# Performance work log

Hardware: AMD Instinct MI355X
Metric: run time of the kernel (lower is better)

## Reference

```python
import jax, jax.numpy as jnp
import numpy as np
import math

BS, LQ, LKV = 4, 2048, 2048
D_LATENT, D_MODEL, HEADS = 512, 512, 8
D_K = D_MODEL // HEADS


def setup_inputs() -> dict:
    key = jax.random.key(0)
    ks = jax.random.split(key, 12)
    s = 0.02
    return {
        "q": jax.random.normal(ks[0], (BS, LQ, D_LATENT), jnp.float32),
        "k": jax.random.normal(ks[1], (BS, LKV, D_MODEL), jnp.float32),
        "v": jax.random.normal(ks[2], (BS, LKV, D_MODEL), jnp.float32),
        "weights": jax.random.uniform(ks[3], (BS, LKV), jnp.float32) + 1e-3,
        "Wq": jax.random.normal(ks[4], (D_LATENT, D_MODEL), jnp.float32) * s,
        "bq": jnp.zeros((D_MODEL,), jnp.float32),
        "Wk": jax.random.normal(ks[5], (D_MODEL, D_MODEL), jnp.float32) * s,
        "bk": jnp.zeros((D_MODEL,), jnp.float32),
        "Wv": jax.random.normal(ks[6], (D_MODEL, D_MODEL), jnp.float32) * s,
        "bv": jnp.zeros((D_MODEL,), jnp.float32),
        "Wo": jax.random.normal(ks[7], (D_MODEL, D_MODEL), jnp.float32) * s,
        "bo": jnp.zeros((D_MODEL,), jnp.float32),
    }


def reference(q, k, v, weights, Wq, bq, Wk, bk, Wv, bv, Wo, bo):
    bs = q.shape[0]
    # QKV projections, split into heads: [bs, h, L, d_k]
    qh = (q @ Wq + bq).reshape(bs, -1, HEADS, D_K).transpose(0, 2, 1, 3)
    kh = (k @ Wk + bk).reshape(bs, -1, HEADS, D_K).transpose(0, 2, 1, 3)
    vh = (v @ Wv + bv).reshape(bs, -1, HEADS, D_K).transpose(0, 2, 1, 3)
    # scaled dot-product scores [bs, h, Lq, Lkv]
    scores = jnp.einsum("bhqd,bhkd->bhqk", qh, kh) / math.sqrt(D_K)
    p = jax.nn.softmax(scores, axis=-1)
    # post-softmax external weight renormalization
    wp = p * weights[:, None, None, :]
    wp = wp / wp.sum(-1, keepdims=True)
    out = jnp.einsum("bhqk,bhkd->bhqd", wp, vh)
    concat = out.transpose(0, 2, 1, 3).reshape(bs, -1, D_MODEL)
    return concat @ Wo + bo
```

## Files before the change

### kernel.cpp

```cpp
#include <hip/hip_runtime.h>
#include <hip/hip_bf16.h>

#define LQ 2048
#define LKV 2048
#define DM 512
#define NH 8
#define DK 64

typedef __attribute__((ext_vector_type(8))) __bf16 bf16x8;
typedef __attribute__((ext_vector_type(4))) float f32x4;
typedef __attribute__((ext_vector_type(16))) float f32x16;

#define AS1 __attribute__((address_space(1)))
#define AS3 __attribute__((address_space(3)))

static __device__ __forceinline__ unsigned short f2bf(float x) {
  unsigned u = __float_as_uint(x);
  return (unsigned short)((u + 0x7fffu + ((u >> 16) & 1u)) >> 16);
}
static __device__ __forceinline__ float bf2f(unsigned short u) {
  return __uint_as_float(((unsigned)u) << 16);
}
static __device__ __forceinline__ bf16x8 cvt8(f32x4 a, f32x4 b) {
  bf16x8 r;
  r[0] = (__bf16)a[0]; r[1] = (__bf16)a[1]; r[2] = (__bf16)a[2]; r[3] = (__bf16)a[3];
  r[4] = (__bf16)b[0]; r[5] = (__bf16)b[1]; r[6] = (__bf16)b[2]; r[7] = (__bf16)b[3];
  return r;
}

__global__ __launch_bounds__(256) void transpose_w(
    const float* __restrict__ Wq, const float* __restrict__ Wk,
    const float* __restrict__ Wv, const float* __restrict__ Wo,
    unsigned short* __restrict__ WtAll)
{
  const float* W = blockIdx.z == 0 ? Wq : blockIdx.z == 1 ? Wk : blockIdx.z == 2 ? Wv : Wo;
  unsigned short* Wt = WtAll + (size_t)blockIdx.z * DM * DM;
  __shared__ float tile[32][33];
  const int t = threadIdx.x;
  const int tr = t >> 3;
  const int tc4 = (t & 7) * 4;
  const int k0 = blockIdx.x * 32, n0 = blockIdx.y * 32;
  float4 v = *(const float4*)(W + (size_t)(k0 + tr) * DM + n0 + tc4);
  tile[tr][tc4 + 0] = v.x; tile[tr][tc4 + 1] = v.y;
  tile[tr][tc4 + 2] = v.z; tile[tr][tc4 + 3] = v.w;
  __syncthreads();
  ushort4 o;
  o.x = f2bf(tile[tc4 + 0][tr]);
  o.y = f2bf(tile[tc4 + 1][tr]);
  o.z = f2bf(tile[tc4 + 2][tr]);
  o.w = f2bf(tile[tc4 + 3][tr]);
  *(ushort4*)(Wt + (size_t)(n0 + tr) * DM + k0 + tc4) = o;
}

__global__ __launch_bounds__(256) void gemm_qkv(
    const float* __restrict__ qin, const float* __restrict__ kin, const float* __restrict__ vin,
    const unsigned short* __restrict__ WtAll,
    const float* __restrict__ bq, const float* __restrict__ bk, const float* __restrict__ bv,
    unsigned short* __restrict__ qh, unsigned short* __restrict__ kh, unsigned short* __restrict__ vh)
{
  const int bid = blockIdx.x;
  const int x = bid & 7, j = bid >> 3;
  const int p = x + 8 * (j >> 2);
  const int nt = j & 3;
  const int mode = p >> 6, mtile = p & 63;

  const float* A = mode == 0 ? qin : (mode == 1 ? kin : vin);
  const unsigned short* Bt = WtAll + (size_t)mode * DM * DM;
  const float* bias = mode == 0 ? bq : (mode == 1 ? bk : bv);
  unsigned short* out = mode == 0 ? qh : (mode == 1 ? kh : vh);
  const float scale = (mode == 0) ? 0.18033688011112042f : 1.0f;

  __shared__ __align__(16) float As[128 * 32];
  __shared__ __align__(16) unsigned short Bs[128 * 32];

  const int tid = threadIdx.x;
  const int lane = tid & 63;
  const int w = tid >> 6;
  const int wr = w >> 1, wc = w & 1;
  const int l15 = lane & 15, g = lane >> 4;
  const int m0 = mtile * 128, n0 = nt * 128;

  f32x4 acc[4][4] = {};

  for (int k0 = 0; k0 < DM; k0 += 32) {
#pragma unroll
    for (int i = 0; i < 4; ++i) {
      int c = tid + i * 256;
      int row = c >> 3, slot = c & 7;
      const float* src = A + (size_t)(m0 + row) * DM + k0 + ((slot ^ (row & 7)) << 2);
      __builtin_amdgcn_global_load_lds((const AS1 unsigned*)src,
                                       (AS3 unsigned*)((char*)As + c * 16), 16, 0, 0);
    }
#pragma unroll
    for (int i = 0; i < 2; ++i) {
      int c = tid + i * 256;
      int row = c >> 2, slot = c & 3;
      const unsigned short* src = Bt + (size_t)(n0 + row) * DM + k0 + ((slot ^ ((row >> 1) & 3)) * 8);
      __builtin_amdgcn_global_load_lds((const AS1 unsigned*)src,
                                       (AS3 unsigned*)((char*)Bs + c * 16), 16, 0, 0);
    }
    __syncthreads();

    bf16x8 af[4], bfr[4];
#pragma unroll
    for (int mi = 0; mi < 4; ++mi) {
      int row = wr * 64 + mi * 16 + l15;
      f32x4 a0 = *(const f32x4*)((const char*)As + row * 128 + (((2 * g) ^ (row & 7)) << 4));
      f32x4 a1 = *(const f32x4*)((const char*)As + row * 128 + (((2 * g + 1) ^ (row & 7)) << 4));
      af[mi] = cvt8(a0, a1);
    }
#pragma unroll
    for (int ni = 0; ni < 4; ++ni) {
      int row = wc * 64 + ni * 16 + l15;
      bfr[ni] = *(const bf16x8*)((const char*)Bs + row * 64 + ((g ^ ((row >> 1) & 3)) * 16));
    }
#pragma unroll
    for (int mi = 0; mi < 4; ++mi)
#pragma unroll
      for (int ni = 0; ni < 4; ++ni)
        acc[mi][ni] = __builtin_amdgcn_mfma_f32_16x16x32_bf16(af[mi], bfr[ni], acc[mi][ni], 0, 0, 0);
    __syncthreads();
  }

#pragma unroll
  for (int mi = 0; mi < 4; ++mi) {
#pragma unroll
    for (int ni = 0; ni < 4; ++ni) {
      int n = n0 + wc * 64 + ni * 16 + l15;
      float bs = bias[n];
      int h = n >> 6, d = n & 63;
#pragma unroll
      for (int r = 0; r < 4; ++r) {
        int m = m0 + wr * 64 + mi * 16 + g * 4 + r;
        int b = m >> 11, li = m & 2047;
        float val = (acc[mi][ni][r] + bs) * scale;
        out[(((size_t)(b * NH + h)) * LQ + li) * DK + d] = f2bf(val);
      }
    }
  }
}

__global__ __launch_bounds__(256) void gemm_out(
    const unsigned short* __restrict__ A, const unsigned short* __restrict__ Bt,
    const float* __restrict__ bias, float* __restrict__ out)
{
  __shared__ __align__(16) unsigned short Al[128 * 40];
  __shared__ __align__(16) unsigned short Bl[128 * 40];
  const int tid = threadIdx.x;
  const int lane = tid & 63;
  const int w = tid >> 6;
  const int wr = w >> 1, wc = w & 1;
  const int l15 = lane & 15, g = lane >> 4;
  const int m0 = blockIdx.x * 128, n0 = blockIdx.y * 128;
  f32x4 acc[4][4] = {};

  for (int k0 = 0; k0 < DM; k0 += 32) {
#pragma unroll
    for (int i = 0; i < 2; ++i) {
      int idx = tid + i * 256;
      int row = idx >> 2, seg = idx & 3;
      *(int4*)(&Al[row * 40 + seg * 8]) =
          *(const int4*)(A + (size_t)(m0 + row) * DM + k0 + seg * 8);
      *(int4*)(&Bl[row * 40 + seg * 8]) =
          *(const int4*)(Bt + (size_t)(n0 + row) * DM + k0 + seg * 8);
    }
    __syncthreads();
    bf16x8 af[4], bfr[4];
#pragma unroll
    for (int mi = 0; mi < 4; ++mi)
      af[mi] = *(const bf16x8*)(&Al[(wr * 64 + mi * 16 + l15) * 40 + g * 8]);
#pragma unroll
    for (int ni = 0; ni < 4; ++ni)
      bfr[ni] = *(const bf16x8*)(&Bl[(wc * 64 + ni * 16 + l15) * 40 + g * 8]);
#pragma unroll
    for (int mi = 0; mi < 4; ++mi)
#pragma unroll
      for (int ni = 0; ni < 4; ++ni)
        acc[mi][ni] = __builtin_amdgcn_mfma_f32_16x16x32_bf16(af[mi], bfr[ni], acc[mi][ni], 0, 0, 0);
    __syncthreads();
  }

#pragma unroll
  for (int mi = 0; mi < 4; ++mi) {
#pragma unroll
    for (int ni = 0; ni < 4; ++ni) {
      int n = n0 + wc * 64 + ni * 16 + l15;
      float bs = bias[n];
#pragma unroll
      for (int r = 0; r < 4; ++r) {
        int m = m0 + wr * 64 + mi * 16 + g * 4 + r;
        out[(size_t)m * DM + n] = acc[mi][ni][r] + bs;
      }
    }
  }
}

__global__ __launch_bounds__(256) void prep_kv(
    const unsigned short* __restrict__ kh, const unsigned short* __restrict__ vh,
    const float* __restrict__ wts,
    unsigned short* __restrict__ kf, unsigned short* __restrict__ vf,
    unsigned short* __restrict__ wbf)
{
  __shared__ __align__(16) unsigned short t[64 * 72];
  const int bh = blockIdx.y, l0 = blockIdx.x * 64;
  const int b = bh >> 3;
  const size_t base = (size_t)bh * LKV * DK;
  const int tid = threadIdx.x;

  if ((bh & 7) == 0 && tid < 64)
    wbf[b * LKV + l0 + tid] = f2bf(wts[b * LKV + l0 + tid]);

#pragma unroll
  for (int i = 0; i < 2; ++i) {
    int c = tid + i * 256;
    int sl = c & 63, cq = (c >> 6) & 3, tl = c >> 8;
    int kv = tl * 32 + (sl & 31);
    int4 blk = *(const int4*)(kh + base + (size_t)(l0 + kv) * DK + cq * 16 + (sl >> 5) * 8);
    *(int4*)(kf + base + ((((size_t)(l0 >> 5) + tl) * 4 + cq) * 64 + sl) * 8) = blk;
  }

#pragma unroll
  for (int i = 0; i < 2; ++i) {
    int idx = tid + i * 256;
    int row = idx >> 3, seg = idx & 7;
    *(int4*)(&t[row * 72 + seg * 8]) =
        *(const int4*)(vh + base + (size_t)(l0 + row) * DK + seg * 8);
  }
  __syncthreads();
#pragma unroll
  for (int i = 0; i < 2; ++i) {
    int idx = tid + i * 256;
    int d = idx >> 3, seg = idx & 7;
    int kvg = l0 + seg * 8;
    float4 wa = *(const float4*)(wts + b * LKV + kvg);
    float4 wb = *(const float4*)(wts + b * LKV + kvg + 4);
    unsigned short r0 = f2bf(wa.x * bf2f(t[(seg * 8 + 0) * 72 + d]));
    unsigned short r1 = f2bf(wa.y * bf2f(t[(seg * 8 + 1) * 72 + d]));
    unsigned short r2 = f2bf(wa.z * bf2f(t[(seg * 8 + 2) * 72 + d]));
    unsigned short r3 = f2bf(wa.w * bf2f(t[(seg * 8 + 3) * 72 + d]));
    unsigned short r4 = f2bf(wb.x * bf2f(t[(seg * 8 + 4) * 72 + d]));
    unsigned short r5 = f2bf(wb.y * bf2f(t[(seg * 8 + 5) * 72 + d]));
    unsigned short r6 = f2bf(wb.z * bf2f(t[(seg * 8 + 6) * 72 + d]));
    unsigned short r7 = f2bf(wb.w * bf2f(t[(seg * 8 + 7) * 72 + d]));
    int4 o;
    o.x = (int)((unsigned)r0 | ((unsigned)r1 << 16));
    o.y = (int)((unsigned)r2 | ((unsigned)r3 << 16));
    o.z = (int)((unsigned)r4 | ((unsigned)r5 << 16));
    o.w = (int)((unsigned)r6 | ((unsigned)r7 << 16));
    size_t addr = ((((size_t)bh * 128 + (kvg >> 4)) * 2 + (d >> 5)) * 64 +
                   ((d & 31) + ((kvg >> 3) & 1) * 32)) * 8;
    *(int4*)(vf + addr) = o;
  }
}

__global__ __launch_bounds__(512, 4) void attn_fwd(
    const unsigned short* __restrict__ qh, const unsigned short* __restrict__ kf,
    const unsigned short* __restrict__ vf, const unsigned short* __restrict__ wbf,
    unsigned short* __restrict__ ao)
{
  const int bid = blockIdx.x;
  const int xcd = bid & 7, wi = bid >> 3;
  const int bh = xcd * 4 + (wi >> 4);
  const int qb = wi & 15;
  const int b = bh >> 3, h = bh & 7;
  const int tid = threadIdx.x, lane = tid & 63, w = tid >> 6;
  const int wq = w & 3, half = w >> 2;
  const int l31 = lane & 31, hi = lane >> 5;

  __shared__ __align__(16) char smem[36864];

  const size_t kv_bh = (size_t)bh * (LKV * DK);
  const unsigned short* kfb = kf + kv_bh;
  const unsigned short* vfb = vf + kv_bh;

  const int q0 = qb * 128 + wq * 32;

#define STAGE(buf, t)                                                                     \
  do {                                                                                    \
    int tg_ = half * 32 + (t);                                                            \
    const unsigned short* ks_ = kfb + ((size_t)(tg_ * 4 + wq) * 64 + lane) * 8;           \
    const unsigned short* vs_ = vfb + ((size_t)((tg_ * 2 + (wq >> 1)) * 2 + (wq & 1)) * 64 + lane) * 8; \
    char* kd_ = smem + (buf) * 16384 + half * 8192 + wq * 1024;                           \
    char* vd_ = smem + (buf) * 16384 + half * 8192 + 4096 + wq * 1024;                    \
    __builtin_amdgcn_global_load_lds((const AS1 unsigned*)ks_, (AS3 unsigned*)kd_, 16, 0, 0); \
    __builtin_amdgcn_global_load_lds((const AS1 unsigned*)vs_, (AS3 unsigned*)vd_, 16, 0, 0); \
  } while (0)

  if (tid < 256)
    __builtin_amdgcn_global_load_lds((const AS1 unsigned*)(wbf + b * LKV + tid * 8),
                                     (AS3 unsigned*)(smem + 32768 + tid * 16), 16, 0, 0);
  STAGE(0, 0);

  bf16x8 qf[4];
  {
    const unsigned short* qp = qh + kv_bh + (size_t)(q0 + l31) * DK + hi * 8;
#pragma unroll
    for (int cq = 0; cq < 4; ++cq) qf[cq] = *(const bf16x8*)(qp + cq * 16);
  }
  asm volatile("s_waitcnt vmcnt(0)" ::: "memory");
  __builtin_amdgcn_s_barrier();

  const char* wl = smem + 32768 + half * 2048;
  f32x16 accO0 = {}, accO1 = {}, accL = {};
  int cur = 0;

#pragma unroll 2
  for (int t = 0; t < 32; ++t) {
    if (t < 31) {
      STAGE(cur ^ 1, t + 1);
      asm volatile("s_waitcnt vmcnt(2)" ::: "memory");
    } else {
      asm volatile("s_waitcnt vmcnt(0)" ::: "memory");
    }
    __builtin_amdgcn_s_barrier();

    const char* Kb = smem + cur * 16384 + half * 8192;
    const char* Vb = Kb + 4096;

    __builtin_amdgcn_s_setprio(1);
    f32x16 s = {};
#pragma unroll
    for (int cq = 0; cq < 4; ++cq) {
      bf16x8 kfr = *(const bf16x8*)(Kb + cq * 1024 + lane * 16);
      s = __builtin_amdgcn_mfma_f32_32x32x16_bf16(kfr, qf[cq], s, 0, 0, 0);
    }

    unsigned D[8];
#pragma unroll
    for (int r2 = 0; r2 < 8; ++r2) {
      float lo = __builtin_amdgcn_exp2f(s[2 * r2]);
      float hv = __builtin_amdgcn_exp2f(s[2 * r2 + 1]);
      __bf16 bl = (__bf16)lo, bh2 = (__bf16)hv;
      unsigned short ul = __builtin_bit_cast(unsigned short, bl);
      unsigned short uh = __builtin_bit_cast(unsigned short, bh2);
      D[r2] = (unsigned)ul | ((unsigned)uh << 16);
    }

    const int kvt = t * 32;
#pragma unroll
    for (int c = 0; c < 2; ++c) {
      bf16x8 vb0 = *(const bf16x8*)(Vb + (c * 2 + 0) * 1024 + lane * 16);
      bf16x8 vb1 = *(const bf16x8*)(Vb + (c * 2 + 1) * 1024 + lane * 16);
      bf16x8 wv8 = *(const bf16x8*)(wl + kvt * 2 + c * 32 + hi * 16);

      int base = 4 * c;
      unsigned s0 = hi ? D[base] : D[base + 2];
      unsigned s1 = hi ? D[base + 1] : D[base + 3];
      unsigned X0 = (unsigned)__shfl_xor((int)s0, 32);
      unsigned X1 = (unsigned)__shfl_xor((int)s1, 32);
      union { unsigned u[4]; bf16x8 v; } pa;
      pa.u[0] = hi ? X0 : D[base];
      pa.u[1] = hi ? X1 : D[base + 1];
      pa.u[2] = hi ? D[base + 2] : X0;
      pa.u[3] = hi ? D[base + 3] : X1;

      bf16x8 z = {};
      bf16x8 wb = (l31 == 0) ? wv8 : z;

      accO0 = __builtin_amdgcn_mfma_f32_32x32x16_bf16(pa.v, vb0, accO0, 0, 0, 0);
      accO1 = __builtin_amdgcn_mfma_f32_32x32x16_bf16(pa.v, vb1, accO1, 0, 0, 0);
      accL  = __builtin_amdgcn_mfma_f32_32x32x16_bf16(pa.v, wb,  accL,  0, 0, 0);
    }
    __builtin_amdgcn_s_setprio(0);

    asm volatile("s_waitcnt lgkmcnt(0)" ::: "memory");
    __builtin_amdgcn_s_barrier();
    cur ^= 1;
  }
#undef STAGE

  float* Ob = (float*)smem;
  float* Lb = (float*)(smem + 34816);
  if (half == 1) {
#pragma unroll
    for (int r = 0; r < 16; ++r) {
      int qp_ = (r & 3) + 8 * (r >> 2) + 4 * hi;
      Ob[(wq * 32 + qp_) * 68 + l31] = accO0[r];
      Ob[(wq * 32 + qp_) * 68 + 32 + l31] = accO1[r];
    }
    if (l31 == 0) {
#pragma unroll
      for (int r = 0; r < 16; ++r) {
        int qp_ = (r & 3) + 8 * (r >> 2) + 4 * hi;
        Lb[wq * 32 + qp_] = accL[r];
      }
    }
  }
  __syncthreads();
  if (half == 0) {
#pragma unroll
    for (int r = 0; r < 16; ++r) {
      int qp_ = (r & 3) + 8 * (r >> 2) + 4 * hi;
      float L = __shfl(accL[r], lane & 32) + Lb[wq * 32 + qp_];
      float inv = 1.0f / L;
      float o0 = accO0[r] + Ob[(wq * 32 + qp_) * 68 + l31];
      float o1 = accO1[r] + Ob[(wq * 32 + qp_) * 68 + 32 + l31];
      size_t off = ((size_t)(b * LQ + q0 + qp_)) * DM + h * DK;
      ao[off + l31] = f2bf(o0 * inv);
      ao[off + 32 + l31] = f2bf(o1 * inv);
    }
  }
}

extern "C" void kernel_launch(void* const* d_in, const int* in_sizes, int n_in,
                              void* d_out, int out_size, void* d_ws, size_t ws_size,
                              hipStream_t stream)
{
  const float* q  = (const float*)d_in[0];
  const float* k  = (const float*)d_in[1];
  const float* v  = (const float*)d_in[2];
  const float* wt = (const float*)d_in[3];
  const float* Wq = (const float*)d_in[4];
  const float* bq = (const float*)d_in[5];
  const float* Wk = (const float*)d_in[6];
  const float* bk = (const float*)d_in[7];
  const float* Wv = (const float*)d_in[8];
  const float* bv = (const float*)d_in[9];
  const float* Wo = (const float*)d_in[10];
  const float* bo = (const float*)d_in[11];

  char* ws = (char*)d_ws;
  unsigned short* qh = (unsigned short*)(ws + 0);
  unsigned short* kfr= (unsigned short*)(ws + 8388608);
  unsigned short* vfr= (unsigned short*)(ws + 16777216);
  unsigned short* ao = (unsigned short*)(ws + 25165824);
  unsigned short* Wt = (unsigned short*)(ws + 33554432);
  unsigned short* vh = (unsigned short*)(ws + 35651584);
  unsigned short* wbf= (unsigned short*)(ws + 44040192);
  unsigned short* kh = ao;

  transpose_w<<<dim3(16, 16, 4), 256, 0, stream>>>(Wq, Wk, Wv, Wo, Wt);
  gemm_qkv<<<768, 256, 0, stream>>>(q, k, v, Wt, bq, bk, bv, qh, kh, vh);
  prep_kv<<<dim3(32, 32), 256, 0, stream>>>(kh, vh, wt, kfr, vfr, wbf);
  attn_fwd<<<512, 512, 0, stream>>>(qh, kfr, vfr, wbf, ao);
  gemm_out<<<dim3(64, 4), 256, 0, stream>>>(ao, Wt + 3 * (size_t)DM * DM, bo, (float*)d_out);
}
```

Measured before the change: 100.0 us.

## Permute V and weight layouts so P fragments feed MFMA without lane shuffles

The V prep kernel now writes its bf16 fragments in a permuted kv order, and the weight vector is stored with a matching index permutation. The S accumulator registers can then be used directly as the A operand of the PV MFMAs, which removes the cross-lane shuffles and selects from the inner loop. The weight operand is chosen by pointer between the real weights and a zeroed LDS pad, which replaces a per-iteration register select. The cost is narrower 8-byte stores in prep_kv and a tight coupling between the layout conventions of the two kernels.

```diff
diff --git a/kernel.cpp b/kernel.cpp
--- a/kernel.cpp
+++ b/kernel.cpp
@@ -207,8 +207,12 @@
   const size_t base = (size_t)bh * LKV * DK;
   const int tid = threadIdx.x;
 
-  if ((bh & 7) == 0 && tid < 64)
-    wbf[b * LKV + l0 + tid] = f2bf(wts[b * LKV + l0 + tid]);
+  if ((bh & 7) == 0 && tid < 64) {
+    int kv = l0 + tid;
+    int r = kv & 15;
+    int p = (r & 3) | ((r & 4) << 1) | ((r & 8) >> 1);
+    wbf[b * LKV + (kv & ~15) + p] = f2bf(wts[b * LKV + kv]);
+  }
 
 #pragma unroll
   for (int i = 0; i < 2; ++i) {
@@ -233,23 +237,22 @@
     int d = idx >> 3, seg = idx & 7;
     int kvg = l0 + seg * 8;
     float4 wa = *(const float4*)(wts + b * LKV + kvg);
-    float4 wb = *(const float4*)(wts + b * LKV + kvg + 4);
+    float4 wb4 = *(const float4*)(wts + b * LKV + kvg + 4);
     unsigned short r0 = f2bf(wa.x * bf2f(t[(seg * 8 + 0) * 72 + d]));
     unsigned short r1 = f2bf(wa.y * bf2f(t[(seg * 8 + 1) * 72 + d]));
     unsigned short r2 = f2bf(wa.z * bf2f(t[(seg * 8 + 2) * 72 + d]));
     unsigned short r3 = f2bf(wa.w * bf2f(t[(seg * 8 + 3) * 72 + d]));
-    unsigned short r4 = f2bf(wb.x * bf2f(t[(seg * 8 + 4) * 72 + d]));
-    unsigned short r5 = f2bf(wb.y * bf2f(t[(seg * 8 + 5) * 72 + d]));
-    unsigned short r6 = f2bf(wb.z * bf2f(t[(seg * 8 + 6) * 72 + d]));
-    unsigned short r7 = f2bf(wb.w * bf2f(t[(seg * 8 + 7) * 72 + d]));
-    int4 o;
-    o.x = (int)((unsigned)r0 | ((unsigned)r1 << 16));
-    o.y = (int)((unsigned)r2 | ((unsigned)r3 << 16));
-    o.z = (int)((unsigned)r4 | ((unsigned)r5 << 16));
-    o.w = (int)((unsigned)r6 | ((unsigned)r7 << 16));
-    size_t addr = ((((size_t)bh * 128 + (kvg >> 4)) * 2 + (d >> 5)) * 64 +
-                   ((d & 31) + ((kvg >> 3) & 1) * 32)) * 8;
-    *(int4*)(vf + addr) = o;
+    unsigned short r4 = f2bf(wb4.x * bf2f(t[(seg * 8 + 4) * 72 + d]));
+    unsigned short r5 = f2bf(wb4.y * bf2f(t[(seg * 8 + 5) * 72 + d]));
+    unsigned short r6 = f2bf(wb4.z * bf2f(t[(seg * 8 + 6) * 72 + d]));
+    unsigned short r7 = f2bf(wb4.w * bf2f(t[(seg * 8 + 7) * 72 + d]));
+    int T = kvg >> 4, s = (kvg >> 3) & 1, dh = d >> 5, dl = d & 31;
+    size_t slot = (((size_t)bh * 128 + T) * 2 + dh) * 64;
+    ushort4 lo4, hi4;
+    lo4.x = r0; lo4.y = r1; lo4.z = r2; lo4.w = r3;
+    hi4.x = r4; hi4.y = r5; hi4.z = r6; hi4.w = r7;
+    *(ushort4*)(vf + (slot + dl) * 8 + 4 * s) = lo4;
+    *(ushort4*)(vf + (slot + dl + 32) * 8 + 4 * s) = hi4;
   }
 }
 
@@ -267,7 +270,7 @@
   const int wq = w & 3, half = w >> 2;
   const int l31 = lane & 31, hi = lane >> 5;
 
-  __shared__ __align__(16) char smem[36864];
+  __shared__ __align__(16) char smem[36928];
 
   const size_t kv_bh = (size_t)bh * (LKV * DK);
   const unsigned short* kfb = kf + kv_bh;
@@ -289,6 +292,7 @@
   if (tid < 256)
     __builtin_amdgcn_global_load_lds((const AS1 unsigned*)(wbf + b * LKV + tid * 8),
                                      (AS3 unsigned*)(smem + 32768 + tid * 16), 16, 0, 0);
+  if (tid < 16) *(int*)(smem + 36864 + tid * 4) = 0;
   STAGE(0, 0);
 
   bf16x8 qf[4];
@@ -297,10 +301,10 @@
 #pragma unroll
     for (int cq = 0; cq < 4; ++cq) qf[cq] = *(const bf16x8*)(qp + cq * 16);
   }
-  asm volatile("s_waitcnt vmcnt(0)" ::: "memory");
-  __builtin_amdgcn_s_barrier();
-
-  const char* wl = smem + 32768 + half * 2048;
+  __syncthreads();
+
+  const char* wl = smem + 32768 + half * 2048 + hi * 16;
+  const char* zpad = smem + 36864;
   f32x16 accO0 = {}, accO1 = {}, accL = {};
   int cur = 0;
 
@@ -325,7 +329,7 @@
       s = __builtin_amdgcn_mfma_f32_32x32x16_bf16(kfr, qf[cq], s, 0, 0, 0);
     }
 
-    unsigned D[8];
+    union { unsigned u[8]; bf16x8 v[2]; } P;
 #pragma unroll
     for (int r2 = 0; r2 < 8; ++r2) {
       float lo = __builtin_amdgcn_exp2f(s[2 * r2]);
@@ -333,33 +337,20 @@
       __bf16 bl = (__bf16)lo, bh2 = (__bf16)hv;
       unsigned short ul = __builtin_bit_cast(unsigned short, bl);
       unsigned short uh = __builtin_bit_cast(unsigned short, bh2);
-      D[r2] = (unsigned)ul | ((unsigned)uh << 16);
-    }
-
-    const int kvt = t * 32;
+      P.u[r2] = (unsigned)ul | ((unsigned)uh << 16);
+    }
+
+    const char* wsel = (l31 == 0) ? (wl + t * 64) : zpad;
+
 #pragma unroll
     for (int c = 0; c < 2; ++c) {
       bf16x8 vb0 = *(const bf16x8*)(Vb + (c * 2 + 0) * 1024 + lane * 16);
       bf16x8 vb1 = *(const bf16x8*)(Vb + (c * 2 + 1) * 1024 + lane * 16);
-      bf16x8 wv8 = *(const bf16x8*)(wl + kvt * 2 + c * 32 + hi * 16);
-
-      int base = 4 * c;
-      unsigned s0 = hi ? D[base] : D[base + 2];
-      unsigned s1 = hi ? D[base + 1] : D[base + 3];
-      unsigned X0 = (unsigned)__shfl_xor((int)s0, 32);
-      unsigned X1 = (unsigned)__shfl_xor((int)s1, 32);
-      union { unsigned u[4]; bf16x8 v; } pa;
-      pa.u[0] = hi ? X0 : D[base];
-      pa.u[1] = hi ? X1 : D[base + 1];
-      pa.u[2] = hi ? D[base + 2] : X0;
-      pa.u[3] = hi ? D[base + 3] : X1;
-
-      bf16x8 z = {};
-      bf16x8 wb = (l31 == 0) ? wv8 : z;
-
-      accO0 = __builtin_amdgcn_mfma_f32_32x32x16_bf16(pa.v, vb0, accO0, 0, 0, 0);
-      accO1 = __builtin_amdgcn_mfma_f32_32x32x16_bf16(pa.v, vb1, accO1, 0, 0, 0);
-      accL  = __builtin_amdgcn_mfma_f32_32x32x16_bf16(pa.v, wb,  accL,  0, 0, 0);
+      bf16x8 wb = *(const bf16x8*)(wsel + c * 32);
+
+      accO0 = __builtin_amdgcn_mfma_f32_32x32x16_bf16(P.v[c], vb0, accO0, 0, 0, 0);
+      accO1 = __builtin_amdgcn_mfma_f32_32x32x16_bf16(P.v[c], vb1, accO1, 0, 0, 0);
+      accL  = __builtin_amdgcn_mfma_f32_32x32x16_bf16(P.v[c], wb,  accL,  0, 0, 0);
     }
     __builtin_amdgcn_s_setprio(0);
 
```

Result: faster. 95.70 us (-4.3%).
